# Performance work log

Hardware: AMD Instinct MI355X
Metric: run time of the kernel (lower is better)

The kernel has to match this reference:

```python
import jax, jax.numpy as jnp
import numpy as np

# icosphere level-6 mesh dims
B, CIN, COUT = 8, 64, 64
NV_PREV, NV, NF = 10242, 40962, 81920


def spmm(x, rows, cols, vals, nrows):
    # x: [..., ncols]; sparse S [nrows, ncols] in COO -> y[..., r] = sum S[r,c] x[..., c]
    out = jnp.zeros(x.shape[:-1] + (nrows,), x.dtype)
    return out.at[..., rows].add(x[..., cols] * vals)


def setup_inputs() -> dict:
    key = jax.random.key(0)
    ks = jax.random.split(key, 12)
    x = jax.random.normal(ks[0], (B, CIN, NV_PREV), jnp.float32)
    # G: per-face gradient operator [3*NF, NV], 3 nnz per row (face vertices)
    G_rows = jnp.repeat(jnp.arange(3 * NF, dtype=jnp.int32), 3)
    G_cols = jax.random.randint(ks[1], (3 * NF * 3,), 0, NV, dtype=jnp.int32)
    G_vals = jax.random.normal(ks[2], (3 * NF * 3,), jnp.float32) * 0.1
    # L: vertex Laplacian [NV, NV], ~7 nnz per row
    L_rows = jnp.repeat(jnp.arange(NV, dtype=jnp.int32), 7)
    L_cols = jax.random.randint(ks[3], (NV * 7,), 0, NV, dtype=jnp.int32)
    L_vals = jax.random.normal(ks[4], (NV * 7,), jnp.float32) * 0.1
    # F2V: face-to-vertex averaging [NV, NF], ~6 nnz per row
    F2V_rows = jnp.repeat(jnp.arange(NV, dtype=jnp.int32), 6)
    F2V_cols = jax.random.randint(ks[5], (NV * 6,), 0, NF, dtype=jnp.int32)
    F2V_vals = jnp.full((NV * 6,), 1.0 / 6.0, jnp.float32)
    # per-face east-west / north-south tangent weights [NF, 3]
    EW = jax.random.normal(ks[6], (NF, 3), jnp.float32)
    NS = jax.random.normal(ks[7], (NF, 3), jnp.float32)
    # learned parameters
    stdv = 1.0 / np.sqrt(CIN * 4)
    coeffs = jax.random.uniform(ks[8], (COUT, CIN, 4), jnp.float32, -stdv, stdv)
    bias = jax.random.uniform(ks[9], (COUT,), jnp.float32, -stdv, stdv)
    return {
        "x": x,
        "G_rows": G_rows, "G_cols": G_cols, "G_vals": G_vals,
        "L_rows": L_rows, "L_cols": L_cols, "L_vals": L_vals,
        "F2V_rows": F2V_rows, "F2V_cols": F2V_cols, "F2V_vals": F2V_vals,
        "EW": EW, "NS": NS, "coeffs": coeffs, "bias": bias,
    }


def reference(x, G_rows, G_cols, G_vals, L_rows, L_cols, L_vals,
              F2V_rows, F2V_cols, F2V_vals, EW, NS, coeffs, bias):
    b, c = x.shape[:2]
    # pad new (upsampled) vertices with ones: [B, C, NV]
    xin = jnp.concatenate([x, jnp.ones((b, c, NV - NV_PREV), x.dtype)], axis=-1)
    # per-face gradient: [B, C, 3*NF] -> [B, C, NF, 3]
    grad_face = spmm(xin, G_rows, G_cols, G_vals, 3 * NF)
    grad_face = grad_face.reshape(b, c, 3, NF).transpose(0, 1, 3, 2)
    # Laplacian: [B, C, NV]
    laplacian = spmm(xin, L_rows, L_cols, L_vals, NV)
    # project face gradients onto EW/NS tangent dirs: [B, C, NF]
    grad_face_ew = jnp.sum(grad_face * EW, axis=-1)
    grad_face_ns = jnp.sum(grad_face * NS, axis=-1)
    # average back to vertices: [B, C, NV]
    grad_vert_ew = spmm(grad_face_ew, F2V_rows, F2V_cols, F2V_vals, NV)
    grad_vert_ns = spmm(grad_face_ns, F2V_rows, F2V_cols, F2V_vals, NV)
    # fuse 4 feature maps with learned coeffs: [B, CIN, NV, 4] x [COUT, CIN, 4]
    feat = jnp.stack([xin, laplacian, grad_vert_ew, grad_vert_ns], axis=-1)
    out = jnp.einsum("bcvk,ock->bov", feat, coeffs) + bias[:, None]
    return out
```

## Files before the change

kernel.cpp:

```cpp
#include <hip/hip_runtime.h>
#include <hip/hip_bf16.h>

typedef __hip_bfloat16 bf16;
typedef __attribute__((ext_vector_type(8))) short short8;
typedef __attribute__((ext_vector_type(4))) float floatx4;

#define NVP 10242
#define NV  40962
#define NF  81920
#define VPB 32
#define FPW 4

__device__ __forceinline__ float bfbits2f(unsigned short u) {
    union { unsigned int i; float f; } cv; cv.i = ((unsigned int)u) << 16;
    return cv.f;
}
__device__ __forceinline__ unsigned short f2bfbits(float f) {
    bf16 h = __float2bfloat16(f);
    return __builtin_bit_cast(unsigned short, h);
}
__device__ __forceinline__ unsigned short pk_fp8(float a, float b) {
    int p = __builtin_amdgcn_cvt_pk_fp8_f32(a, b, 0, false);
    return (unsigned short)(p & 0xffff);
}
__device__ __forceinline__ unsigned char one_fp8(float a) {
    int p = __builtin_amdgcn_cvt_pk_fp8_f32(a, 0.f, 0, false);
    return (unsigned char)(p & 0xff);
}
__device__ __forceinline__ float fp8_lo(unsigned int u) {
    return __builtin_amdgcn_cvt_f32_fp8(u, 0);
}
__device__ __forceinline__ float fp8_hi(unsigned int u) {
    return __builtin_amdgcn_cvt_f32_fp8(u, 1);
}

__global__ void k_coeffsB(const float* __restrict__ coeffs,
                          unsigned short* __restrict__ coeffsB) {
    int t = blockIdx.x * 256 + threadIdx.x;
    int j = t & 7, lane = (t >> 3) & 63, s = t >> 9;
    int ot = s >> 3, kk = s & 7;
    int o  = ot * 16 + (lane & 15);
    int kg = kk * 32 + (lane >> 4) * 8 + j;
    coeffsB[t] = f2bfbits(coeffs[o * 256 + kg]);
}

__global__ void k_packG(const int* __restrict__ G_cols,
                        const float* __restrict__ G_vals,
                        const float* __restrict__ EW,
                        const float* __restrict__ NS,
                        float* __restrict__ Gpk) {
    int f = blockIdx.x * 256 + threadIdx.x;
    float r[32];
#pragma unroll
    for (int q = 0; q < 32; ++q) r[q] = 0.f;
#pragma unroll
    for (int d = 0; d < 3; ++d)
#pragma unroll
        for (int j = 0; j < 3; ++j) {
            int idx = (d * NF + f) * 3 + j;
            r[d * 3 + j]      = __int_as_float(G_cols[idx]);
            r[16 + d * 3 + j] = G_vals[idx];
        }
#pragma unroll
    for (int d = 0; d < 3; ++d) {
        r[25 + d] = EW[f * 3 + d];
        r[28 + d] = NS[f * 3 + d];
    }
    float4* dst = (float4*)(Gpk + (size_t)f * 32);
#pragma unroll
    for (int q = 0; q < 8; ++q) dst[q] = ((const float4*)r)[q];
}

__global__ void k_packV(const int* __restrict__ L_cols,
                        const float* __restrict__ L_vals,
                        const int* __restrict__ F2V_cols,
                        const float* __restrict__ F2V_vals,
                        float* __restrict__ Vpk) {
    int v = blockIdx.x * 256 + threadIdx.x;
    if (v >= NV) return;
    float r[32];
#pragma unroll
    for (int q = 0; q < 32; ++q) r[q] = 0.f;
#pragma unroll
    for (int j = 0; j < 7; ++j) {
        r[j]      = __int_as_float(L_cols[v * 7 + j]);
        r[16 + j] = L_vals[v * 7 + j];
    }
#pragma unroll
    for (int j = 0; j < 6; ++j) {
        r[8 + j]  = __int_as_float(F2V_cols[v * 6 + j]);
        r[24 + j] = F2V_vals[v * 6 + j];
    }
    float4* dst = (float4*)(Vpk + (size_t)v * 32);
#pragma unroll
    for (int q = 0; q < 8; ++q) dst[q] = ((const float4*)r)[q];
}

__global__ void k_transpose(const float* __restrict__ x,
                            unsigned short* __restrict__ xin,
                            unsigned char* __restrict__ xin8) {
    x    += (size_t)blockIdx.y * 64 * NVP;
    xin  += (size_t)blockIdx.y * 64 * NV;
    xin8 += (size_t)blockIdx.y * 64 * NV;
    __shared__ float tile[64][65];
    int v0 = blockIdx.x * 64;
    int tx = threadIdx.x & 63;
    int ty = threadIdx.x >> 6;
    int v  = v0 + tx;
#pragma unroll
    for (int r = 0; r < 16; ++r) {
        int c = ty + r * 4;
        tile[tx][c] = (v < NVP) ? x[c * NVP + v] : 1.0f;
    }
    __syncthreads();
#pragma unroll
    for (int r = 0; r < 16; ++r) {
        int vl = ty + r * 4;
        int vv = v0 + vl;
        if (vv < NV) {
            float val = tile[vl][tx];
            xin [vv * 64 + tx] = f2bfbits(val);
            xin8[vv * 64 + tx] = one_fp8(val);
        }
    }
}

__global__ void __launch_bounds__(256, 4) k_facegrad(
    const unsigned char* __restrict__ xin8,
    const float* __restrict__ Gpk,
    unsigned short* __restrict__ gfi) {
    xin8 += (size_t)blockIdx.y * 64 * NV;
    gfi  += (size_t)blockIdx.y * 64 * NF;
    int w  = __builtin_amdgcn_readfirstlane(threadIdx.x >> 6);
    int c  = threadIdx.x & 63;
    int f0 = (blockIdx.x * 4 + w) * FPW;
    float xv[FPW][9];
#pragma unroll
    for (int i = 0; i < FPW; ++i) {
        const unsigned int* ru = (const unsigned int*)(Gpk + (size_t)(f0 + i) * 32);
#pragma unroll
        for (int j = 0; j < 9; ++j) {
            int col = (int)ru[j];
            xv[i][j] = fp8_lo((unsigned int)xin8[col * 64 + c]);
        }
    }
#pragma unroll
    for (int i = 0; i < FPW; ++i) {
        const float* rf = Gpk + (size_t)(f0 + i) * 32;
        float g0 = rf[16] * xv[i][0] + rf[17] * xv[i][1] + rf[18] * xv[i][2];
        float g1 = rf[19] * xv[i][3] + rf[20] * xv[i][4] + rf[21] * xv[i][5];
        float g2 = rf[22] * xv[i][6] + rf[23] * xv[i][7] + rf[24] * xv[i][8];
        float ew = g0 * rf[25] + g1 * rf[26] + g2 * rf[27];
        float ns = g0 * rf[28] + g1 * rf[29] + g2 * rf[30];
        gfi[(f0 + i) * 64 + c] = pk_fp8(ew, ns);
    }
}

__global__ void __launch_bounds__(512) k_vertex(
    const unsigned short* __restrict__ xin,
    const unsigned char* __restrict__ xin8,
    const float* __restrict__ Vpk,
    const unsigned short* __restrict__ gfi,
    const unsigned short* __restrict__ coeffsB,
    const float* __restrict__ bias,
    float* __restrict__ out) {
    xin  += (size_t)blockIdx.y * 64 * NV;
    xin8 += (size_t)blockIdx.y * 64 * NV;
    gfi  += (size_t)blockIdx.y * 64 * NF;
    out  += (size_t)blockIdx.y * 64 * NV;
    int vb = blockIdx.x * VPB;

    __shared__ unsigned short feat[VPB * 264];
    __shared__ float outs[VPB * 65];
    int w    = __builtin_amdgcn_readfirstlane(threadIdx.x >> 6);
    int lane = threadIdx.x & 63;
    int c    = lane;

    int   vcs[4];
    float f0v[4], lap[4], ewا[4], ns_[4];
#pragma unroll
    for (int i = 0; i < 4; ++i) {
        int v = vb + w * 4 + i;
        vcs[i] = __builtin_amdgcn_readfirstlane(v < NV ? v : NV - 1);
    }
#pragma unroll
    for (int i = 0; i < 4; ++i) {
        const float* rf = Vpk + (size_t)vcs[i] * 32;
        const unsigned int* ru = (const unsigned int*)rf;
        f0v[i] = bfbits2f(xin[vcs[i] * 64 + c]);
        float l = 0.f;
#pragma unroll
        for (int j = 0; j < 7; ++j) {
            int col = (int)ru[j];
            l += rf[16 + j] * fp8_lo((unsigned int)xin8[col * 64 + c]);
        }
        lap[i] = l;
        float e = 0.f, n = 0.f;
#pragma unroll
        for (int j = 0; j < 6; ++j) {
            int   col = (int)ru[8 + j];
            float val = rf[24 + j];
            unsigned int u = gfi[col * 64 + c];
            e += val * fp8_lo(u);
            n += val * fp8_hi(u);
        }
        ewا[i] = e; ns_[i] = n;
    }
#pragma unroll
    for (int i = 0; i < 4; ++i) {
        int vloc = w * 4 + i;
        ushort4 p = make_ushort4(f2bfbits(f0v[i]), f2bfbits(lap[i]),
                                 f2bfbits(ewا[i]), f2bfbits(ns_[i]));
        *(ushort4*)&feat[vloc * 264 + c * 4] = p;
    }
    __syncthreads();

    int m = lane & 15, quad = lane >> 4;
    int ot = w & 3, vh = w >> 2;
    float bo = bias[ot * 16 + m];
    floatx4 acc = {bo, bo, bo, bo};
#pragma unroll
    for (int kk = 0; kk < 8; ++kk) {
        short8 a = *(const short8*)&feat[(vh * 16 + m) * 264 + kk * 32 + quad * 8];
        short8 bfr = *(const short8*)&coeffsB[((ot * 8 + kk) * 64 + lane) * 8];
        acc = __builtin_amdgcn_mfma_f32_16x16x32_bf16(a, bfr, acc, 0, 0, 0);
    }

#pragma unroll
    for (int r = 0; r < 4; ++r)
        outs[(vh * 16 + quad * 4 + r) * 65 + ot * 16 + m] = acc[r];
    __syncthreads();
    int vp = threadIdx.x & 31;
    int og = threadIdx.x >> 5;
    if (vb + vp < NV) {
#pragma unroll
        for (int r = 0; r < 4; ++r) {
            int o2 = og + r * 16;
            out[(size_t)o2 * NV + vb + vp] = outs[vp * 65 + o2];
        }
    }
}

extern "C" void kernel_launch(void* const* d_in, const int* in_sizes, int n_in,
                              void* d_out, int out_size, void* d_ws, size_t ws_size,
                              hipStream_t stream) {
    const float* x        = (const float*)d_in[0];
    const int*   G_cols   = (const int*)  d_in[2];
    const float* G_vals   = (const float*)d_in[3];
    const int*   L_cols   = (const int*)  d_in[5];
    const float* L_vals   = (const float*)d_in[6];
    const int*   F2V_cols = (const int*)  d_in[8];
    const float* F2V_vals = (const float*)d_in[9];
    const float* EW       = (const float*)d_in[10];
    const float* NS       = (const float*)d_in[11];
    const float* coeffs   = (const float*)d_in[12];
    const float* bias     = (const float*)d_in[13];
    float* out = (float*)d_out;

    char* ws = (char*)d_ws;
    const size_t xin_b = (size_t)NV * 64;
    const size_t gf_b  = (size_t)NF * 64;
    const size_t gpk_bytes = (size_t)NF * 128;
    const size_t vpk_bytes = (size_t)NV * 128;
    const size_t fixed = 65536 + gpk_bytes + vpk_bytes;
    size_t perb = 2 * xin_b + 2 * gf_b + xin_b;
    int nb = (ws_size >= fixed + 8 * perb) ? 8
           : (ws_size >= fixed + 2 * perb) ? 2 : 1;

    unsigned short* coeffsB = (unsigned short*)ws;
    float* Gpk = (float*)(ws + 65536);
    float* Vpk = Gpk + (size_t)NF * 32;
    unsigned short* xin  = (unsigned short*)(ws + fixed);
    unsigned short* gfi  = xin + (size_t)nb * xin_b;
    unsigned char*  xin8 = (unsigned char*)(gfi + (size_t)nb * gf_b);

    k_coeffsB<<<64, 256, 0, stream>>>(coeffs, coeffsB);
    k_packG<<<NF / 256, 256, 0, stream>>>(G_cols, G_vals, EW, NS, Gpk);
    k_packV<<<(NV + 255) / 256, 256, 0, stream>>>(L_cols, L_vals,
                                                  F2V_cols, F2V_vals, Vpk);
    for (int b0 = 0; b0 < 8; b0 += nb) {
        dim3 gt(641, nb), gg(NF / (4 * FPW), nb), gv((NV + VPB - 1) / VPB, nb);
        k_transpose<<<gt, 256, 0, stream>>>(x + (size_t)b0 * 64 * NVP, xin, xin8);
        k_facegrad<<<gg, 256, 0, stream>>>(xin8, Gpk, gfi);
        k_vertex<<<gv, 512, 0, stream>>>(xin, xin8, Vpk, gfi, coeffsB, bias,
                                         out + (size_t)b0 * 64 * NV);
    }
}
```

Before: 347.0 us.

## Fuse prep kernels, interleave batches in grid, batch gather loads for more parallelism

Merges the three one-time packing kernels into one launch, saving two launch overheads. The face-gradient and vertex kernels now put the batch index in the low bits of a 1D block index, so blocks that run close together use the same index rows and different batches. Both kernels load all gather indices first and then issue every gathered load before any arithmetic, which raises memory-level parallelism. The vertex kernel also gets a min-blocks launch bound of 2 and passes the bf16 self feature through unchanged; the extra live registers could cost occupancy.

```diff
diff --git a/kernel.cpp b/kernel.cpp
--- a/kernel.cpp
+++ b/kernel.cpp
@@ -34,66 +34,67 @@
     return __builtin_amdgcn_cvt_f32_fp8(u, 1);
 }
 
-__global__ void k_coeffsB(const float* __restrict__ coeffs,
-                          unsigned short* __restrict__ coeffsB) {
-    int t = blockIdx.x * 256 + threadIdx.x;
-    int j = t & 7, lane = (t >> 3) & 63, s = t >> 9;
-    int ot = s >> 3, kk = s & 7;
-    int o  = ot * 16 + (lane & 15);
-    int kg = kk * 32 + (lane >> 4) * 8 + j;
-    coeffsB[t] = f2bfbits(coeffs[o * 256 + kg]);
-}
-
-__global__ void k_packG(const int* __restrict__ G_cols,
-                        const float* __restrict__ G_vals,
-                        const float* __restrict__ EW,
-                        const float* __restrict__ NS,
-                        float* __restrict__ Gpk) {
-    int f = blockIdx.x * 256 + threadIdx.x;
-    float r[32];
-#pragma unroll
-    for (int q = 0; q < 32; ++q) r[q] = 0.f;
-#pragma unroll
-    for (int d = 0; d < 3; ++d)
-#pragma unroll
-        for (int j = 0; j < 3; ++j) {
-            int idx = (d * NF + f) * 3 + j;
-            r[d * 3 + j]      = __int_as_float(G_cols[idx]);
-            r[16 + d * 3 + j] = G_vals[idx];
-        }
-#pragma unroll
-    for (int d = 0; d < 3; ++d) {
-        r[25 + d] = EW[f * 3 + d];
-        r[28 + d] = NS[f * 3 + d];
-    }
-    float4* dst = (float4*)(Gpk + (size_t)f * 32);
-#pragma unroll
-    for (int q = 0; q < 8; ++q) dst[q] = ((const float4*)r)[q];
-}
-
-__global__ void k_packV(const int* __restrict__ L_cols,
-                        const float* __restrict__ L_vals,
-                        const int* __restrict__ F2V_cols,
-                        const float* __restrict__ F2V_vals,
-                        float* __restrict__ Vpk) {
-    int v = blockIdx.x * 256 + threadIdx.x;
-    if (v >= NV) return;
-    float r[32];
-#pragma unroll
-    for (int q = 0; q < 32; ++q) r[q] = 0.f;
-#pragma unroll
-    for (int j = 0; j < 7; ++j) {
-        r[j]      = __int_as_float(L_cols[v * 7 + j]);
-        r[16 + j] = L_vals[v * 7 + j];
-    }
-#pragma unroll
-    for (int j = 0; j < 6; ++j) {
-        r[8 + j]  = __int_as_float(F2V_cols[v * 6 + j]);
-        r[24 + j] = F2V_vals[v * 6 + j];
-    }
-    float4* dst = (float4*)(Vpk + (size_t)v * 32);
-#pragma unroll
-    for (int q = 0; q < 8; ++q) dst[q] = ((const float4*)r)[q];
+__global__ void k_prep(const float* __restrict__ coeffs,
+                       unsigned short* __restrict__ coeffsB,
+                       const int* __restrict__ G_cols,
+                       const float* __restrict__ G_vals,
+                       const float* __restrict__ EW,
+                       const float* __restrict__ NS,
+                       float* __restrict__ Gpk,
+                       const int* __restrict__ L_cols,
+                       const float* __restrict__ L_vals,
+                       const int* __restrict__ F2V_cols,
+                       const float* __restrict__ F2V_vals,
+                       float* __restrict__ Vpk) {
+    int b = blockIdx.x;
+    if (b < 64) {
+        int t = b * 256 + threadIdx.x;
+        int j = t & 7, lane = (t >> 3) & 63, s = t >> 9;
+        int ot = s >> 3, kk = s & 7;
+        int o  = ot * 16 + (lane & 15);
+        int kg = kk * 32 + (lane >> 4) * 8 + j;
+        coeffsB[t] = f2bfbits(coeffs[o * 256 + kg]);
+    } else if (b < 384) {
+        int f = (b - 64) * 256 + threadIdx.x;
+        float r[32];
+#pragma unroll
+        for (int q = 0; q < 32; ++q) r[q] = 0.f;
+#pragma unroll
+        for (int d = 0; d < 3; ++d)
+#pragma unroll
+            for (int j = 0; j < 3; ++j) {
+                int idx = (d * NF + f) * 3 + j;
+                r[d * 3 + j]      = __int_as_float(G_cols[idx]);
+                r[16 + d * 3 + j] = G_vals[idx];
+            }
+#pragma unroll
+        for (int d = 0; d < 3; ++d) {
+            r[25 + d] = EW[f * 3 + d];
+            r[28 + d] = NS[f * 3 + d];
+        }
+        float4* dst = (float4*)(Gpk + (size_t)f * 32);
+#pragma unroll
+        for (int q = 0; q < 8; ++q) dst[q] = ((const float4*)r)[q];
+    } else {
+        int v = (b - 384) * 256 + threadIdx.x;
+        if (v >= NV) return;
+        float r[32];
+#pragma unroll
+        for (int q = 0; q < 32; ++q) r[q] = 0.f;
+#pragma unroll
+        for (int j = 0; j < 7; ++j) {
+            r[j]      = __int_as_float(L_cols[v * 7 + j]);
+            r[16 + j] = L_vals[v * 7 + j];
+        }
+#pragma unroll
+        for (int j = 0; j < 6; ++j) {
+            r[8 + j]  = __int_as_float(F2V_cols[v * 6 + j]);
+            r[24 + j] = F2V_vals[v * 6 + j];
+        }
+        float4* dst = (float4*)(Vpk + (size_t)v * 32);
+#pragma unroll
+        for (int q = 0; q < 8; ++q) dst[q] = ((const float4*)r)[q];
+    }
 }
 
 __global__ void k_transpose(const float* __restrict__ x,
@@ -128,47 +129,58 @@
 __global__ void __launch_bounds__(256, 4) k_facegrad(
     const unsigned char* __restrict__ xin8,
     const float* __restrict__ Gpk,
-    unsigned short* __restrict__ gfi) {
-    xin8 += (size_t)blockIdx.y * 64 * NV;
-    gfi  += (size_t)blockIdx.y * 64 * NF;
+    unsigned short* __restrict__ gfi, int nbm, int nbs) {
+    int batch = blockIdx.x & nbm;
+    int fblk  = blockIdx.x >> nbs;
+    xin8 += (size_t)batch * 64 * NV;
+    gfi  += (size_t)batch * 64 * NF;
     int w  = __builtin_amdgcn_readfirstlane(threadIdx.x >> 6);
     int c  = threadIdx.x & 63;
-    int f0 = (blockIdx.x * 4 + w) * FPW;
-    float xv[FPW][9];
+    int f0 = (fblk * 4 + w) * FPW;
+
+    int gc[FPW][9];
 #pragma unroll
     for (int i = 0; i < FPW; ++i) {
-        const unsigned int* ru = (const unsigned int*)(Gpk + (size_t)(f0 + i) * 32);
-#pragma unroll
-        for (int j = 0; j < 9; ++j) {
-            int col = (int)ru[j];
-            xv[i][j] = fp8_lo((unsigned int)xin8[col * 64 + c]);
-        }
-    }
+        const int* ri = (const int*)(Gpk + (size_t)(f0 + i) * 32);
+#pragma unroll
+        for (int j = 0; j < 9; ++j) gc[i][j] = ri[j];
+    }
+    unsigned int xv[FPW][9];
+#pragma unroll
+    for (int i = 0; i < FPW; ++i)
+#pragma unroll
+        for (int j = 0; j < 9; ++j)
+            xv[i][j] = xin8[(size_t)gc[i][j] * 64 + c];
 #pragma unroll
     for (int i = 0; i < FPW; ++i) {
         const float* rf = Gpk + (size_t)(f0 + i) * 32;
-        float g0 = rf[16] * xv[i][0] + rf[17] * xv[i][1] + rf[18] * xv[i][2];
-        float g1 = rf[19] * xv[i][3] + rf[20] * xv[i][4] + rf[21] * xv[i][5];
-        float g2 = rf[22] * xv[i][6] + rf[23] * xv[i][7] + rf[24] * xv[i][8];
+        float g0 = rf[16] * fp8_lo(xv[i][0]) + rf[17] * fp8_lo(xv[i][1])
+                 + rf[18] * fp8_lo(xv[i][2]);
+        float g1 = rf[19] * fp8_lo(xv[i][3]) + rf[20] * fp8_lo(xv[i][4])
+                 + rf[21] * fp8_lo(xv[i][5]);
+        float g2 = rf[22] * fp8_lo(xv[i][6]) + rf[23] * fp8_lo(xv[i][7])
+                 + rf[24] * fp8_lo(xv[i][8]);
         float ew = g0 * rf[25] + g1 * rf[26] + g2 * rf[27];
         float ns = g0 * rf[28] + g1 * rf[29] + g2 * rf[30];
         gfi[(f0 + i) * 64 + c] = pk_fp8(ew, ns);
     }
 }
 
-__global__ void __launch_bounds__(512) k_vertex(
+__global__ void __launch_bounds__(512, 2) k_vertex(
     const unsigned short* __restrict__ xin,
     const unsigned char* __restrict__ xin8,
     const float* __restrict__ Vpk,
     const unsigned short* __restrict__ gfi,
     const unsigned short* __restrict__ coeffsB,
     const float* __restrict__ bias,
-    float* __restrict__ out) {
-    xin  += (size_t)blockIdx.y * 64 * NV;
-    xin8 += (size_t)blockIdx.y * 64 * NV;
-    gfi  += (size_t)blockIdx.y * 64 * NF;
-    out  += (size_t)blockIdx.y * 64 * NV;
-    int vb = blockIdx.x * VPB;
+    float* __restrict__ out,
+    int nbm, int nbs) {
+    int batch = blockIdx.x & nbm;
+    int vb    = (blockIdx.x >> nbs) * VPB;
+    xin  += (size_t)batch * 64 * NV;
+    xin8 += (size_t)batch * 64 * NV;
+    gfi  += (size_t)batch * 64 * NF;
+    out  += (size_t)batch * 64 * NV;
 
     __shared__ unsigned short feat[VPB * 264];
     __shared__ float outs[VPB * 65];
@@ -176,42 +188,49 @@
     int lane = threadIdx.x & 63;
     int c    = lane;
 
-    int   vcs[4];
-    float f0v[4], lap[4], ewا[4], ns_[4];
+    int vcs[4];
 #pragma unroll
     for (int i = 0; i < 4; ++i) {
         int v = vb + w * 4 + i;
         vcs[i] = __builtin_amdgcn_readfirstlane(v < NV ? v : NV - 1);
     }
+    int lc[4][7], fc[4][6];
 #pragma unroll
     for (int i = 0; i < 4; ++i) {
-        const float* rf = Vpk + (size_t)vcs[i] * 32;
-        const unsigned int* ru = (const unsigned int*)rf;
-        f0v[i] = bfbits2f(xin[vcs[i] * 64 + c]);
-        float l = 0.f;
-#pragma unroll
-        for (int j = 0; j < 7; ++j) {
-            int col = (int)ru[j];
-            l += rf[16 + j] * fp8_lo((unsigned int)xin8[col * 64 + c]);
-        }
-        lap[i] = l;
-        float e = 0.f, n = 0.f;
+        const int* ri = (const int*)(Vpk + (size_t)vcs[i] * 32);
+#pragma unroll
+        for (int j = 0; j < 7; ++j) lc[i][j] = ri[j];
+#pragma unroll
+        for (int j = 0; j < 6; ++j) fc[i][j] = ri[8 + j];
+    }
+    unsigned int f0u[4], xl[4][7], gg[4][6];
+#pragma unroll
+    for (int i = 0; i < 4; ++i) {
+        f0u[i] = xin[(size_t)vcs[i] * 64 + c];
+#pragma unroll
+        for (int j = 0; j < 7; ++j)
+            xl[i][j] = xin8[(size_t)lc[i][j] * 64 + c];
+#pragma unroll
+        for (int j = 0; j < 6; ++j)
+            gg[i][j] = gfi[(size_t)fc[i][j] * 64 + c];
+    }
+#pragma unroll
+    for (int i = 0; i < 4; ++i) {
+        const float* rv = Vpk + (size_t)vcs[i] * 32;
+        float lap = 0.f;
+#pragma unroll
+        for (int j = 0; j < 7; ++j)
+            lap += rv[16 + j] * fp8_lo(xl[i][j]);
+        float ew = 0.f, ns = 0.f;
 #pragma unroll
         for (int j = 0; j < 6; ++j) {
-            int   col = (int)ru[8 + j];
-            float val = rf[24 + j];
-            unsigned int u = gfi[col * 64 + c];
-            e += val * fp8_lo(u);
-            n += val * fp8_hi(u);
-        }
-        ewا[i] = e; ns_[i] = n;
-    }
-#pragma unroll
-    for (int i = 0; i < 4; ++i) {
-        int vloc = w * 4 + i;
-        ushort4 p = make_ushort4(f2bfbits(f0v[i]), f2bfbits(lap[i]),
-                                 f2bfbits(ewا[i]), f2bfbits(ns_[i]));
-        *(ushort4*)&feat[vloc * 264 + c * 4] = p;
+            float val = rv[24 + j];
+            ew += val * fp8_lo(gg[i][j]);
+            ns += val * fp8_hi(gg[i][j]);
+        }
+        ushort4 p = make_ushort4((unsigned short)f0u[i], f2bfbits(lap),
+                                 f2bfbits(ew), f2bfbits(ns));
+        *(ushort4*)&feat[(w * 4 + i) * 264 + c * 4] = p;
     }
     __syncthreads();
 
@@ -266,6 +285,7 @@
     size_t perb = 2 * xin_b + 2 * gf_b + xin_b;
     int nb = (ws_size >= fixed + 8 * perb) ? 8
            : (ws_size >= fixed + 2 * perb) ? 2 : 1;
+    int nbs = (nb == 8) ? 3 : (nb == 2) ? 1 : 0;
 
     unsigned short* coeffsB = (unsigned short*)ws;
     float* Gpk = (float*)(ws + 65536);
@@ -274,15 +294,17 @@
     unsigned short* gfi  = xin + (size_t)nb * xin_b;
     unsigned char*  xin8 = (unsigned char*)(gfi + (size_t)nb * gf_b);
 
-    k_coeffsB<<<64, 256, 0, stream>>>(coeffs, coeffsB);
-    k_packG<<<NF / 256, 256, 0, stream>>>(G_cols, G_vals, EW, NS, Gpk);
-    k_packV<<<(NV + 255) / 256, 256, 0, stream>>>(L_cols, L_vals,
-                                                  F2V_cols, F2V_vals, Vpk);
+    k_prep<<<545, 256, 0, stream>>>(coeffs, coeffsB, G_cols, G_vals, EW, NS,
+                                    Gpk, L_cols, L_vals, F2V_cols, F2V_vals,
+                                    Vpk);
+    const int nvb = (NV + VPB - 1) / VPB;
+    const int nfb = NF / (4 * FPW);
     for (int b0 = 0; b0 < 8; b0 += nb) {
-        dim3 gt(641, nb), gg(NF / (4 * FPW), nb), gv((NV + VPB - 1) / VPB, nb);
+        dim3 gt(641, nb);
         k_transpose<<<gt, 256, 0, stream>>>(x + (size_t)b0 * 64 * NVP, xin, xin8);
-        k_facegrad<<<gg, 256, 0, stream>>>(xin8, Gpk, gfi);
-        k_vertex<<<gv, 512, 0, stream>>>(xin, xin8, Vpk, gfi, coeffsB, bias,
-                                         out + (size_t)b0 * 64 * NV);
-    }
-}
+        k_facegrad<<<nfb * nb, 256, 0, stream>>>(xin8, Gpk, gfi, nb - 1, nbs);
+        k_vertex<<<nvb * nb, 512, 0, stream>>>(xin, xin8, Vpk, gfi, coeffsB,
+                                               bias, out + (size_t)b0 * 64 * NV,
+                                               nb - 1, nbs);
+    }
+}
```

New measurement: 308.4 us. 11.1% less time.
